# Performance work log

Measured on AMD Instinct MI355X. Metric: run time of the kernel, lower is better.

The kernel has to match this reference:

```python
import jax, jax.numpy as jnp
import numpy as np

H, D, K, FF = 4, 256, 1024, 1024  # n_head, d_model, key_feature_dim, dim_feedforward
L, B = 2048, 4                    # pixels, batch


def setup_inputs() -> dict:
    key = jax.random.key(0)
    ks = jax.random.split(key, 12)
    def g(k, shape, s=0.02):
        return jax.random.normal(k, shape, jnp.float32) * s
    return dict(
        src=jax.random.normal(ks[0], (L, B, D), jnp.float32),
        WK=g(ks[1], (H, K, D), (2.0 / K) ** 0.5),
        WQ=g(ks[2], (H, K, D), (2.0 / K) ** 0.5),
        WV=g(ks[3], (H, D, D), (2.0 / D) ** 0.5),
        TC=g(ks[4], (H, D, D)),
        ENw1=g(ks[5], (H, FF, D)), ENb1=jnp.zeros((H, FF), jnp.float32),
        ENw2=g(ks[6], (H, D, FF)), ENb2=jnp.zeros((H, D), jnp.float32),
        ENg=jnp.ones((H, D), jnp.float32), ENbeta=jnp.zeros((H, D), jnp.float32),
        Wout=g(ks[7], (D, H * D)),
        L1w=g(ks[8], (FF, D)), L1b=jnp.zeros((FF,), jnp.float32),
        L2w=g(ks[9], (D, FF)), L2b=jnp.zeros((D,), jnp.float32),
        N1g=jnp.ones((D,), jnp.float32), N1b=jnp.zeros((D,), jnp.float32),
        N2g=jnp.ones((D,), jnp.float32), N2b=jnp.zeros((D,), jnp.float32),
    )


def _ln(x, g, b, eps=1e-5):
    m = jnp.mean(x, -1, keepdims=True)
    v = jnp.mean((x - m) ** 2, -1, keepdims=True)
    return (x - m) * jax.lax.rsqrt(v + eps) * g + b


def _l2n(x, eps=1e-12):
    n = jnp.sqrt(jnp.sum(x * x, -1, keepdims=True))
    return x / jnp.maximum(n, eps)


def reference(src, WK, WQ, WV, TC, ENw1, ENb1, ENw2, ENb2, ENg, ENbeta,
              Wout, L1w, L1b, L2w, L2b, N1g, N1b, N2g, N2b):
    # --- RMA: per-head RelationUnit, vectorized over head axis h ---
    wq = _l2n(jnp.einsum('lbd,hkd->hlbk', src, WQ))   # (H,L,B,K), L2-normed
    wk = _l2n(jnp.einsum('lbd,hkd->hlbk', src, WK))
    wv = jnp.einsum('lbd,hed->hlbe', src, WV)         # (H,L,B,D)
    dot = jnp.einsum('hlbk,hmbk->hblm', wq, wk)       # (H,B,Lq,Lk)
    aff = jax.nn.softmax(dot, axis=-1)                 # softmax over keys (temp=1)
    aff = aff / (1e-9 + jnp.sum(aff, axis=2, keepdims=True))  # renorm over QUERY dim (torch dim=1)
    out = jnp.einsum('hblm,hmbe->hlbe', aff, wv)       # (H,L,B,D)
    ru = jax.nn.relu(jnp.einsum('hlbe,hfe->hlbf', src[None] - out, TC))
    # per-head extra TransNonlinear: residual MLP + layernorm
    hid = jax.nn.relu(jnp.einsum('hlbd,hfd->hlbf', ru, ENw1) + ENb1[:, None, None, :])
    s2 = jnp.einsum('hlbf,hdf->hlbd', hid, ENw2) + ENb2[:, None, None, :]
    tn = _ln(ru + s2, ENg[:, None, None, :], ENbeta[:, None, None, :])  # (H,L,B,D)
    concat = jnp.transpose(tn, (1, 2, 0, 3)).reshape(L, B, H * D)
    attn = concat @ Wout.T                              # (L,B,D)
    # --- encoder layer: residual + LN + FFN + LN (dropout = eval identity) ---
    x = _ln(src + attn, N1g, N1b)
    ff = jax.nn.relu(x @ L1w.T + L1b) @ L2w.T + L2b
    return _ln(x + ff, N2g, N2b)
```

## Files before the change

kernel.cpp:

```cpp
#include <hip/hip_runtime.h>
#include <hip/hip_bf16.h>

typedef __hip_bfloat16 bf16;
typedef short s16x8 __attribute__((ext_vector_type(8)));
typedef float f32x4 __attribute__((ext_vector_type(4)));

#ifndef __has_builtin
#define __has_builtin(x) 0
#endif
#if __has_builtin(__builtin_amdgcn_global_load_lds)
#define HAS_GLL 1
#else
#define HAS_GLL 0
#endif

#define HN 4
#define DM 256
#define KF 1024
#define FFD 1024
#define LL 2048
#define BB 4
#define NN (LL * BB)
#define HD (HN * DM)

__device__ __forceinline__ float b2f(unsigned short u) {
    unsigned v = ((unsigned)u) << 16; float f; __builtin_memcpy(&f, &v, 4); return f;
}
__device__ __forceinline__ unsigned short f2b(float f) {
    bf16 b = (bf16)f; unsigned short u; __builtin_memcpy(&u, &b, 2); return u;
}

__device__ __forceinline__ float waveReduceSum(float v) {
    for (int o = 32; o; o >>= 1) v += __shfl_down(v, o, 64);
    return v;
}
__device__ __forceinline__ float waveReduceMax(float v) {
    for (int o = 32; o; o >>= 1) v = fmaxf(v, __shfl_down(v, o, 64));
    return v;
}
__device__ __forceinline__ float blockReduceSum(float v) {
    __shared__ float sh[4];
    v = waveReduceSum(v);
    __syncthreads();
    if ((threadIdx.x & 63) == 0) sh[threadIdx.x >> 6] = v;
    __syncthreads();
    return sh[0] + sh[1] + sh[2] + sh[3];
}
__device__ __forceinline__ float blockReduceMax(float v) {
    __shared__ float sh[4];
    v = waveReduceMax(v);
    __syncthreads();
    if ((threadIdx.x & 63) == 0) sh[threadIdx.x >> 6] = v;
    __syncthreads();
    return fmaxf(fmaxf(sh[0], sh[1]), fmaxf(sh[2], sh[3]));
}

__global__ void sentinel_kernel(float* out, float val) {
    if (threadIdx.x == 0 && blockIdx.x == 0) out[0] = val;
}

#if HAS_GLL
__device__ __forceinline__ void gll16(void* g, void* l) {
    __builtin_amdgcn_global_load_lds(
        (__attribute__((address_space(1))) unsigned int*)g,
        (__attribute__((address_space(3))) unsigned int*)l, 16, 0, 0);
}
#endif

template<int BN>
__global__ __launch_bounds__(256) void gemm_nt(
    const void* __restrict__ A, int aF32, int lda, long sA,
    const void* __restrict__ Bv, int bF32, int ldb, long sB,
    void* __restrict__ C, int cF32, int ldc, long sC,
    int Kc,
    const float* __restrict__ bias, long sBias,
    const void* __restrict__ aux, int auxType, int ldaux, long sAux,
    float accSign, int relu)
{
    constexpr int NI = BN / 32;
    constexpr int WN = BN / 2;
    const int z = blockIdx.z;
    const float* Af = (const float*)A + (long)z * sA;
    const bf16*  Ah = (const bf16*)A + (long)z * sA;
    const float* Bf = (const float*)Bv + (long)z * sB;
    const bf16*  Bh = (const bf16*)Bv + (long)z * sB;
    float* Cf = (float*)C + (long)z * sC;
    bf16*  Ch = (bf16*)C + (long)z * sC;
    const float* biasp = bias ? (bias + (long)z * sBias) : nullptr;
    const float* auxf = (auxType == 1) ? ((const float*)aux + (long)z * sAux) : nullptr;
    const bf16*  auxh = (auxType == 2) ? ((const bf16*)aux + (long)z * sAux) : nullptr;

    __shared__ __align__(16) bf16 As[2][128 * 32];
    __shared__ __align__(16) bf16 Bs[2][BN * 32];

    const int tid = threadIdx.x;
    const int lane = tid & 63;
    const int wv = __builtin_amdgcn_readfirstlane(tid >> 6);
    const int wm = (tid >> 6) & 1;
    const int wn = (tid >> 6) >> 1;
    const int lrow = lane & 15;
    const int quad = lane >> 4;
    const int m0 = blockIdx.x * 128;
    const int n0 = blockIdx.y * BN;
    const int srow = tid >> 1;
    const int scol = (tid & 1) * 16;
    const int drow = wv * 16 + (lane >> 2);
    const int dcol = (lane & 3) * 8;

    f32x4 acc[4][NI] = {};

#if HAS_GLL
    if (!aF32 && !bF32) {
        const int nk = Kc >> 5;
        auto stage = [&](int k0, int buf) {
            const bf16* a0 = Ah + (long)(m0 + drow) * lda + k0 + dcol;
            gll16((void*)a0, (void*)&As[buf][wv * 512]);
            gll16((void*)(a0 + (long)lda * 64), (void*)&As[buf][2048 + wv * 512]);
            const bf16* b0 = Bh + (long)(n0 + drow) * ldb + k0 + dcol;
            gll16((void*)b0, (void*)&Bs[buf][wv * 512]);
            if (BN == 128)
                gll16((void*)(b0 + (long)ldb * 64), (void*)&Bs[buf][2048 + wv * 512]);
        };
        stage(0, 0);
        __syncthreads();
        int cur = 0;
        for (int t = 0; t < nk; ++t) {
            if (t + 1 < nk) stage((t + 1) << 5, cur ^ 1);
            s16x8 af[4], bfg[NI];
#pragma unroll
            for (int mi = 0; mi < 4; mi++)
                af[mi] = *(const s16x8*)&As[cur][(wm * 64 + mi * 16 + lrow) * 32 + quad * 8];
#pragma unroll
            for (int ni = 0; ni < NI; ni++)
                bfg[ni] = *(const s16x8*)&Bs[cur][(wn * WN + ni * 16 + lrow) * 32 + quad * 8];
#pragma unroll
            for (int mi = 0; mi < 4; mi++)
#pragma unroll
                for (int ni = 0; ni < NI; ni++)
                    acc[mi][ni] = __builtin_amdgcn_mfma_f32_16x16x32_bf16(af[mi], bfg[ni], acc[mi][ni], 0, 0, 0);
            __syncthreads();
            cur ^= 1;
        }
    } else
#endif
    {
        for (int k0 = 0; k0 < Kc; k0 += 32) {
            uint4 av0, av1, bv0, bv1;
            if (aF32) {
                const float* ag = Af + (long)(m0 + srow) * lda + k0 + scol;
                ushort t[16];
#pragma unroll
                for (int j = 0; j < 4; j++) {
                    float4 f = *(const float4*)(ag + 4 * j);
                    t[4*j] = f2b(f.x); t[4*j+1] = f2b(f.y); t[4*j+2] = f2b(f.z); t[4*j+3] = f2b(f.w);
                }
                av0 = *(const uint4*)&t[0]; av1 = *(const uint4*)&t[8];
            }
#if !HAS_GLL
            else {
                const bf16* ag = Ah + (long)(m0 + srow) * lda + k0 + scol;
                av0 = *(const uint4*)ag; av1 = *(const uint4*)(ag + 8);
            }
#endif
            if (bF32) {
                if (srow < BN) {
                    const float* bg = Bf + (long)(n0 + srow) * ldb + k0 + scol;
                    ushort t[16];
#pragma unroll
                    for (int j = 0; j < 4; j++) {
                        float4 f = *(const float4*)(bg + 4 * j);
                        t[4*j] = f2b(f.x); t[4*j+1] = f2b(f.y); t[4*j+2] = f2b(f.z); t[4*j+3] = f2b(f.w);
                    }
                    bv0 = *(const uint4*)&t[0]; bv1 = *(const uint4*)&t[8];
                }
            }
#if !HAS_GLL
            else {
                if (srow < BN) {
                    const bf16* bg = Bh + (long)(n0 + srow) * ldb + k0 + scol;
                    bv0 = *(const uint4*)bg; bv1 = *(const uint4*)(bg + 8);
                }
            }
#endif
            __syncthreads();
            if (aF32) {
                *(uint4*)&As[0][srow * 32 + scol] = av0;
                *(uint4*)&As[0][srow * 32 + scol + 8] = av1;
            } else {
#if HAS_GLL
                gll16((void*)(Ah + (long)(m0 + drow) * lda + k0 + dcol), (void*)&As[0][wv * 512]);
                gll16((void*)(Ah + (long)(m0 + 64 + drow) * lda + k0 + dcol), (void*)&As[0][2048 + wv * 512]);
#else
                *(uint4*)&As[0][srow * 32 + scol] = av0;
                *(uint4*)&As[0][srow * 32 + scol + 8] = av1;
#endif
            }
            if (bF32) {
                if (srow < BN) {
                    *(uint4*)&Bs[0][srow * 32 + scol] = bv0;
                    *(uint4*)&Bs[0][srow * 32 + scol + 8] = bv1;
                }
            } else {
#if HAS_GLL
                gll16((void*)(Bh + (long)(n0 + drow) * ldb + k0 + dcol), (void*)&Bs[0][wv * 512]);
                if (BN == 128)
                    gll16((void*)(Bh + (long)(n0 + 64 + drow) * ldb + k0 + dcol), (void*)&Bs[0][2048 + wv * 512]);
#else
                if (srow < BN) {
                    *(uint4*)&Bs[0][srow * 32 + scol] = bv0;
                    *(uint4*)&Bs[0][srow * 32 + scol + 8] = bv1;
                }
#endif
            }
            __syncthreads();

            s16x8 af[4], bfg[NI];
#pragma unroll
            for (int mi = 0; mi < 4; mi++)
                af[mi] = *(const s16x8*)&As[0][(wm * 64 + mi * 16 + lrow) * 32 + quad * 8];
#pragma unroll
            for (int ni = 0; ni < NI; ni++)
                bfg[ni] = *(const s16x8*)&Bs[0][(wn * WN + ni * 16 + lrow) * 32 + quad * 8];
#pragma unroll
            for (int mi = 0; mi < 4; mi++)
#pragma unroll
                for (int ni = 0; ni < NI; ni++)
                    acc[mi][ni] = __builtin_amdgcn_mfma_f32_16x16x32_bf16(af[mi], bfg[ni], acc[mi][ni], 0, 0, 0);
        }
    }

#pragma unroll
    for (int mi = 0; mi < 4; mi++) {
#pragma unroll
        for (int ni = 0; ni < NI; ni++) {
            int col = n0 + wn * WN + ni * 16 + lrow;
            float bvl = biasp ? biasp[col] : 0.0f;
#pragma unroll
            for (int i = 0; i < 4; i++) {
                int row = m0 + wm * 64 + mi * 16 + quad * 4 + i;
                float v = accSign * acc[mi][ni][i] + bvl;
                if (auxType == 1) v += auxf[(long)row * ldaux + col];
                else if (auxType == 2) v += (float)auxh[(long)row * ldaux + col];
                if (relu) v = fmaxf(v, 0.0f);
                if (cF32) Cf[(long)row * ldc + col] = v;
                else Ch[(long)row * ldc + col] = (bf16)v;
            }
        }
    }
}

__global__ __launch_bounds__(256) void cvt4(const float* __restrict__ in, bf16* __restrict__ out, int n4) {
    int i = blockIdx.x * 256 + threadIdx.x;
    if (i < n4) {
        float4 f = ((const float4*)in)[i];
        ushort4 u; u.x = f2b(f.x); u.y = f2b(f.y); u.z = f2b(f.z); u.w = f2b(f.w);
        ((ushort4*)out)[i] = u;
    }
}

struct WCvt {
    const float* in[9];
    bf16* out[9];
    int n4[9];
};
__global__ __launch_bounds__(256) void cvt_weights(WCvt wc) {
    int t = blockIdx.y;
    int n4 = wc.n4[t];
    const float4* in = (const float4*)wc.in[t];
    ushort4* out = (ushort4*)wc.out[t];
    for (int i = blockIdx.x * 256 + threadIdx.x; i < n4; i += gridDim.x * 256) {
        float4 f = in[i];
        ushort4 u; u.x = f2b(f.x); u.y = f2b(f.y); u.z = f2b(f.z); u.w = f2b(f.w);
        out[i] = u;
    }
}

__global__ __launch_bounds__(256) void l2norm_rows(bf16* __restrict__ Q) {
    bf16* q = Q + (long)blockIdx.x * KF;
    ushort4 u = ((ushort4*)q)[threadIdx.x];
    float v0 = b2f(u.x), v1 = b2f(u.y), v2 = b2f(u.z), v3 = b2f(u.w);
    float ss = blockReduceSum(v0 * v0 + v1 * v1 + v2 * v2 + v3 * v3);
    float inv = 1.0f / fmaxf(sqrtf(ss), 1e-12f);
    u.x = f2b(v0 * inv); u.y = f2b(v1 * inv); u.z = f2b(v2 * inv); u.w = f2b(v3 * inv);
    ((ushort4*)q)[threadIdx.x] = u;
}

__global__ __launch_bounds__(256) void softmax_rows(bf16* __restrict__ P) {
    bf16* p = P + (long)blockIdx.x * LL;
    ushort4 a = ((ushort4*)p)[2 * threadIdx.x];
    ushort4 b = ((ushort4*)p)[2 * threadIdx.x + 1];
    float v[8] = {b2f(a.x), b2f(a.y), b2f(a.z), b2f(a.w), b2f(b.x), b2f(b.y), b2f(b.z), b2f(b.w)};
    float mx = -1e30f;
#pragma unroll
    for (int i = 0; i < 8; i++) mx = fmaxf(mx, v[i]);
    mx = blockReduceMax(mx);
    float s = 0.0f;
#pragma unroll
    for (int i = 0; i < 8; i++) { v[i] = __expf(v[i] - mx); s += v[i]; }
    s = blockReduceSum(s);
    float inv = 1.0f / s;
    a.x = f2b(v[0]*inv); a.y = f2b(v[1]*inv); a.z = f2b(v[2]*inv); a.w = f2b(v[3]*inv);
    b.x = f2b(v[4]*inv); b.y = f2b(v[5]*inv); b.z = f2b(v[6]*inv); b.w = f2b(v[7]*inv);
    ((ushort4*)p)[2 * threadIdx.x] = a;
    ((ushort4*)p)[2 * threadIdx.x + 1] = b;
}

__global__ __launch_bounds__(256) void zero_cs(float* __restrict__ cs) {
    cs[blockIdx.x * 256 + threadIdx.x] = 0.0f;
}

__global__ __launch_bounds__(256) void colsum2(const bf16* __restrict__ P, float* __restrict__ cs) {
    int col = blockIdx.x * 256 + threadIdx.x;
    int rc = blockIdx.y;
    int b = blockIdx.z;
    const bf16* p = P + (long)b * LL * LL + (long)rc * 128 * LL + col;
    float s = 0.0f;
#pragma unroll 4
    for (int r = 0; r < 128; r++) s += (float)p[(long)r * LL];
    atomicAdd(&cs[(long)b * LL + col], s);
}

__global__ __launch_bounds__(256) void scale_vt(bf16* __restrict__ vt, const float* __restrict__ cs) {
    int e = blockIdx.x, b = blockIdx.y;
    bf16* row = vt + ((long)b * DM + e) * LL;
    const float* c = cs + (long)b * LL;
#pragma unroll
    for (int i = 0; i < 8; i++) {
        int m = threadIdx.x + i * 256;
        row[m] = (bf16)((float)row[m] / (1e-9f + c[m]));
    }
}

__global__ __launch_bounds__(256) void ln_rows(const bf16* __restrict__ in, void* __restrict__ out,
                                               int outF32,
                                               const float* __restrict__ g, const float* __restrict__ b,
                                               const float* __restrict__ aux) {
    long base = (long)blockIdx.x * 256;
    float v = (float)in[base + threadIdx.x];
    if (aux) v += aux[base + threadIdx.x];
    float mean = blockReduceSum(v) * (1.0f / 256.0f);
    float d = v - mean;
    float var = blockReduceSum(d * d) * (1.0f / 256.0f);
    float o = d * rsqrtf(var + 1e-5f) * g[threadIdx.x] + b[threadIdx.x];
    if (outF32) ((float*)out)[base + threadIdx.x] = o;
    else ((bf16*)out)[base + threadIdx.x] = (bf16)o;
}

__global__ __launch_bounds__(256) void ln_cat(bf16* __restrict__ cat, const float* __restrict__ g,
                                              const float* __restrict__ bb) {
    long n = blockIdx.x;
    int h = blockIdx.y;
    bf16* x = cat + n * HD + (long)h * DM;
    float v = (float)x[threadIdx.x];
    float mean = blockReduceSum(v) * (1.0f / 256.0f);
    float d = v - mean;
    float var = blockReduceSum(d * d) * (1.0f / 256.0f);
    x[threadIdx.x] = (bf16)(d * rsqrtf(var + 1e-5f) * g[h * DM + threadIdx.x] + bb[h * DM + threadIdx.x]);
}

extern "C" void kernel_launch(void* const* d_in, const int* in_sizes, int n_in,
                              void* d_out, int out_size, void* d_ws, size_t ws_size,
                              hipStream_t stream) {
    const float* src  = (const float*)d_in[0];
    const float* WK   = (const float*)d_in[1];
    const float* WQ   = (const float*)d_in[2];
    const float* WV   = (const float*)d_in[3];
    const float* TC   = (const float*)d_in[4];
    const float* ENw1 = (const float*)d_in[5];
    const float* ENb1 = (const float*)d_in[6];
    const float* ENw2 = (const float*)d_in[7];
    const float* ENb2 = (const float*)d_in[8];
    const float* ENg  = (const float*)d_in[9];
    const float* ENbt = (const float*)d_in[10];
    const float* Wout = (const float*)d_in[11];
    const float* L1w  = (const float*)d_in[12];
    const float* L1b  = (const float*)d_in[13];
    const float* L2w  = (const float*)d_in[14];
    const float* L2b  = (const float*)d_in[15];
    const float* N1g  = (const float*)d_in[16];
    const float* N1b  = (const float*)d_in[17];
    const float* N2g  = (const float*)d_in[18];
    const float* N2b  = (const float*)d_in[19];

    const size_t COMPACT_FLOOR = 34700000;
    const size_t FAST_FLOOR  = 92307456;
    const size_t FASTW_FLOOR = 92307456 + 11010048;
    if (ws_size < COMPACT_FLOOR || out_size != NN * DM || n_in != 20) {
        float val;
        if (n_in != 20) val = 32768.0f + (float)n_in;
        else if (out_size != NN * DM) val = 49152.0f;
        else val = 16384.0f + 128.0f * (float)(unsigned)(ws_size >> 20);
        sentinel_kernel<<<1, 64, 0, stream>>>((float*)d_out, val);
        return;
    }

    char* w = (char*)d_ws;
    auto G = [&](const void* A, int aF, int lda, long sA,
                 const void* B, int bF, int ldb, long sB,
                 void* C, int cF, int ldc, long sC,
                 int M, int Nn, int Kc, int nb,
                 const float* bias, long sBias,
                 const void* aux, int auxT, int ldaux, long sAux,
                 float sgn, int relu) {
        gemm_nt<128><<<dim3(M / 128, Nn / 128, nb), dim3(256), 0, stream>>>(
            A, aF, lda, sA, B, bF, ldb, sB, C, cF, ldc, sC, Kc,
            bias, sBias, aux, auxT, ldaux, sAux, sgn, relu);
    };
    auto G64 = [&](const void* A, int aF, int lda, long sA,
                 const void* B, int bF, int ldb, long sB,
                 void* C, int cF, int ldc, long sC,
                 int M, int Nn, int Kc, int nb,
                 const float* bias, long sBias,
                 const void* aux, int auxT, int ldaux, long sAux,
                 float sgn, int relu) {
        gemm_nt<64><<<dim3(M / 128, Nn / 64, nb), dim3(256), 0, stream>>>(
            A, aF, lda, sA, B, bF, ldb, sB, C, cF, ldc, sC, Kc,
            bias, sBias, aux, auxT, ldaux, sAux, sgn, relu);
    };

    if (ws_size >= FAST_FLOOR) {
        bf16*  Sb  = (bf16*)(w + 0);
        bf16*  Q   = (bf16*)(w + 4194304);
        bf16*  K   = (bf16*)(w + 20971520);
        bf16*  Vt  = (bf16*)(w + 37748736);
        bf16*  P   = (bf16*)(w + 41943040);
        bf16*  Su  = (bf16*)(w + 75497472);
        float* Cs  = (float*)(w + 92274688);
        bf16* Ru = Q; bf16* Hid = K; bf16* Cat = P;
        bf16* Attn = Vt; bf16* Xln = Su; bf16* Ffh = Q; bf16* Yp = Vt;

        const int haveWb = (ws_size >= FASTW_FLOOR) ? 1 : 0;
        char* wb = w + 92307456;
        bf16* WKb   = (bf16*)(wb + 0);
        bf16* WQb   = (bf16*)(wb + 2097152);
        bf16* WVb   = (bf16*)(wb + 4194304);
        bf16* TCb   = (bf16*)(wb + 4718592);
        bf16* ENw1b = (bf16*)(wb + 5242880);
        bf16* ENw2b = (bf16*)(wb + 7340032);
        bf16* Woutb = (bf16*)(wb + 9437184);
        bf16* L1wb  = (bf16*)(wb + 9961472);
        bf16* L2wb  = (bf16*)(wb + 10485760);
        if (haveWb) {
            WCvt wc;
            wc.in[0] = WK;   wc.out[0] = WKb;   wc.n4[0] = 262144;
            wc.in[1] = WQ;   wc.out[1] = WQb;   wc.n4[1] = 262144;
            wc.in[2] = WV;   wc.out[2] = WVb;   wc.n4[2] = 65536;
            wc.in[3] = TC;   wc.out[3] = TCb;   wc.n4[3] = 65536;
            wc.in[4] = ENw1; wc.out[4] = ENw1b; wc.n4[4] = 262144;
            wc.in[5] = ENw2; wc.out[5] = ENw2b; wc.n4[5] = 262144;
            wc.in[6] = Wout; wc.out[6] = Woutb; wc.n4[6] = 65536;
            wc.in[7] = L1w;  wc.out[7] = L1wb;  wc.n4[7] = 65536;
            wc.in[8] = L2w;  wc.out[8] = L2wb;  wc.n4[8] = 65536;
            cvt_weights<<<dim3(256, 9), 256, 0, stream>>>(wc);
        }
        const int wF = haveWb ? 0 : 1;
        auto WP = [&](const void* f32p, const void* b16p, long off) {
            return haveWb ? (const void*)((const bf16*)b16p + off)
                          : (const void*)((const float*)f32p + off);
        };

        cvt4<<<2048, 256, 0, stream>>>(src, Sb, NN * DM / 4);

        for (int h = 0; h < HN; h++) {
            G(Sb, 0, DM, 0, WP(WQ, WQb, (long)h * KF * DM), wF, DM, 0, Q, 0, KF, 0,
              NN, KF, DM, 1, nullptr, 0, nullptr, 0, 0, 0, 1.0f, 0);
            G(Sb, 0, DM, 0, WP(WK, WKb, (long)h * KF * DM), wF, DM, 0, K, 0, KF, 0,
              NN, KF, DM, 1, nullptr, 0, nullptr, 0, 0, 0, 1.0f, 0);
            G64(WP(WV, WVb, (long)h * DM * DM), wF, DM, 0, Sb, 0, BB * DM, DM,
              Vt, 0, LL, (long)DM * LL,
              DM, LL, DM, BB, nullptr, 0, nullptr, 0, 0, 0, 1.0f, 0);
            l2norm_rows<<<NN, 256, 0, stream>>>(Q);
            l2norm_rows<<<NN, 256, 0, stream>>>(K);
            G(Q, 0, BB * KF, KF, K, 0, BB * KF, KF, P, 0, LL, (long)LL * LL,
              LL, LL, KF, BB, nullptr, 0, nullptr, 0, 0, 0, 1.0f, 0);
            softmax_rows<<<BB * LL, 256, 0, stream>>>(P);
            zero_cs<<<BB * LL / 256, 256, 0, stream>>>(Cs);
            colsum2<<<dim3(LL / 256, 16, BB), 256, 0, stream>>>(P, Cs);
            scale_vt<<<dim3(DM, BB), 256, 0, stream>>>(Vt, Cs);
            G64(P, 0, LL, (long)LL * LL, Vt, 0, LL, (long)DM * LL,
              Su + (long)h * NN * DM, 0, BB * DM, DM,
              LL, DM, LL, BB, nullptr, 0, Sb, 2, BB * DM, DM, -1.0f, 0);
        }
        G(Su, 0, DM, (long)NN * DM, WP(TC, TCb, 0), wF, DM, (long)DM * DM,
          Ru, 0, DM, (long)NN * DM,
          NN, DM, DM, HN, nullptr, 0, nullptr, 0, 0, 0, 1.0f, 1);
        for (int h = 0; h < HN; h++) {
            G(Ru + (long)h * NN * DM, 0, DM, 0, WP(ENw1, ENw1b, (long)h * FFD * DM), wF, DM, 0,
              Hid, 0, FFD, 0, NN, FFD, DM, 1, ENb1 + (long)h * FFD, 0, nullptr, 0, 0, 0, 1.0f, 1);
            G64(Hid, 0, FFD, 0, WP(ENw2, ENw2b, (long)h * DM * FFD), wF, FFD, 0,
              Cat + (long)h * DM, 0, HD, 0, NN, DM, FFD, 1,
              ENb2 + (long)h * DM, 0, Ru + (long)h * NN * DM, 2, DM, 0, 1.0f, 0);
        }
        ln_cat<<<dim3(NN, HN), 256, 0, stream>>>(Cat, ENg, ENbt);
        G64(Cat, 0, HD, 0, WP(Wout, Woutb, 0), wF, HD, 0, Attn, 0, DM, 0,
          NN, DM, HD, 1, nullptr, 0, nullptr, 0, 0, 0, 1.0f, 0);
        ln_rows<<<NN, 256, 0, stream>>>(Attn, Xln, 0, N1g, N1b, src);
        G(Xln, 0, DM, 0, WP(L1w, L1wb, 0), wF, DM, 0, Ffh, 0, FFD, 0,
          NN, FFD, DM, 1, L1b, 0, nullptr, 0, 0, 0, 1.0f, 1);
        G64(Ffh, 0, FFD, 0, WP(L2w, L2wb, 0), wF, FFD, 0, Yp, 0, DM, 0,
          NN, DM, FFD, 1, L2b, 0, Xln, 2, DM, 0, 1.0f, 0);
        ln_rows<<<NN, 256, 0, stream>>>(Yp, (float*)d_out, 1, N2g, N2b, nullptr);
    } else {
        bf16*  S0 = (bf16*)(w + 0);
        bf16*  S1 = (bf16*)(w + 16777216);
        bf16*  S2 = (bf16*)(w + 20971520);
        bf16*  S3 = (bf16*)(w + 25165824);
        bf16*  S4 = (bf16*)(w + 26214400);
        bf16*  S5 = (bf16*)(w + 30408704);
        float* Cs = (float*)(w + 34603008);

        for (int h = 0; h < HN; h++) {
            for (int b = 0; b < BB; b++) {
                G(src + b * DM, 1, BB * DM, 0, WQ + (long)h * KF * DM, 1, DM, 0,
                  S1, 0, KF, 0, LL, KF, DM, 1, nullptr, 0, nullptr, 0, 0, 0, 1.0f, 0);
                G(src + b * DM, 1, BB * DM, 0, WK + (long)h * KF * DM, 1, DM, 0,
                  S2, 0, KF, 0, LL, KF, DM, 1, nullptr, 0, nullptr, 0, 0, 0, 1.0f, 0);
                G(WV + (long)h * DM * DM, 1, DM, 0, src + b * DM, 1, BB * DM, 0,
                  S3, 0, LL, 0, DM, LL, DM, 1, nullptr, 0, nullptr, 0, 0, 0, 1.0f, 0);
                l2norm_rows<<<LL, 256, 0, stream>>>(S1);
                l2norm_rows<<<LL, 256, 0, stream>>>(S2);
                G(S1, 0, KF, 0, S2, 0, KF, 0, S0, 0, LL, 0,
                  LL, LL, KF, 1, nullptr, 0, nullptr, 0, 0, 0, 1.0f, 0);
                softmax_rows<<<LL, 256, 0, stream>>>(S0);
                zero_cs<<<LL / 256, 256, 0, stream>>>(Cs);
                colsum2<<<dim3(LL / 256, 16, 1), 256, 0, stream>>>(S0, Cs);
                scale_vt<<<dim3(DM, 1), 256, 0, stream>>>(S3, Cs);
                G(S0, 0, LL, 0, S3, 0, LL, 0, S4 + b * DM, 0, BB * DM, 0,
                  LL, DM, LL, 1, nullptr, 0, src + b * DM, 1, BB * DM, 0, -1.0f, 0);
            }
            G(S4, 0, DM, 0, TC + (long)h * DM * DM, 1, DM, 0, S1, 0, DM, 0,
              NN, DM, DM, 1, nullptr, 0, nullptr, 0, 0, 0, 1.0f, 1);
            G(S1, 0, DM, 0, ENw1 + (long)h * FFD * DM, 1, DM, 0, S0, 0, FFD, 0,
              NN, FFD, DM, 1, ENb1 + (long)h * FFD, 0, nullptr, 0, 0, 0, 1.0f, 1);
            G(S0, 0, FFD, 0, ENw2 + (long)h * DM * FFD, 1, FFD, 0, S2, 0, DM, 0,
              NN, DM, FFD, 1, ENb2 + (long)h * DM, 0, S1, 2, DM, 0, 1.0f, 0);
            ln_rows<<<NN, 256, 0, stream>>>(S2, S2, 0, ENg + (long)h * DM, ENbt + (long)h * DM, nullptr);
            G(S2, 0, DM, 0, Wout + (long)h * DM, 1, HD, 0, S5, 0, DM, 0,
              NN, DM, DM, 1, nullptr, 0, (h == 0) ? nullptr : (const void*)S5,
              (h == 0) ? 0 : 2, DM, 0, 1.0f, 0);
        }
        ln_rows<<<NN, 256, 0, stream>>>(S5, S1, 0, N1g, N1b, src);
        G(S1, 0, DM, 0, L1w, 1, DM, 0, S0, 0, FFD, 0,
          NN, FFD, DM, 1, L1b, 0, nullptr, 0, 0, 0, 1.0f, 1);
        G(S0, 0, FFD, 0, L2w, 1, FFD, 0, S2, 0, DM, 0,
          NN, DM, FFD, 1, L2b, 0, S1, 2, DM, 0, 1.0f, 0);
        ln_rows<<<NN, 256, 0, stream>>>(S2, (float*)d_out, 1, N2g, N2b, nullptr);
    }
}
```

Measured before the change: 1.140 ms.

## Add 256x256-tile bf16 MFMA GEMM with direct-to-LDS loads for large GEMMs

Adds a new 512-thread GEMM kernel that computes 256x256 output tiles. It stages A and B straight into swizzled LDS with global_load_lds, double-buffers the K loop and interleaves staging with four MFMA phases under s_setprio. The Q/K projections, the QK^T attention-score GEMM, the TC, ENw1 and L1 GEMMs now use it when bf16 weights are available. The aim is more data reuse per tile and better overlap of loads with compute. In exchange it needs 128 KB of LDS per block, which limits occupancy to one block per CU, and it assumes M and N are multiples of 256 and K is a multiple of 64.

```diff
diff --git a/kernel.cpp b/kernel.cpp
--- a/kernel.cpp
+++ b/kernel.cpp
@@ -64,6 +64,186 @@
     __builtin_amdgcn_global_load_lds(
         (__attribute__((address_space(1))) unsigned int*)g,
         (__attribute__((address_space(3))) unsigned int*)l, 16, 0, 0);
+}
+#endif
+
+#define VMC(n) asm volatile("s_waitcnt vmcnt(" #n ")" ::: "memory")
+#define LGKM0() asm volatile("s_waitcnt lgkmcnt(0)" ::: "memory")
+
+#if HAS_GLL
+__global__ __launch_bounds__(512) void gemm256(
+    const bf16* __restrict__ A, int lda, long sA,
+    const bf16* __restrict__ Bv, int ldb, long sB,
+    void* __restrict__ C, int cF32, int ldc, long sC,
+    int Kc,
+    const float* __restrict__ bias, long sBias,
+    const void* __restrict__ aux, int auxType, int ldaux, long sAux,
+    float accSign, int relu)
+{
+    const int z = blockIdx.z;
+    const bf16* Ah = A + (long)z * sA;
+    const bf16* Bh = Bv + (long)z * sB;
+    float* Cf = (float*)C + (long)z * sC;
+    bf16*  Ch = (bf16*)C + (long)z * sC;
+    const float* biasp = bias ? (bias + (long)z * sBias) : nullptr;
+    const float* auxf = (auxType == 1) ? ((const float*)aux + (long)z * sAux) : nullptr;
+    const bf16*  auxh = (auxType == 2) ? ((const bf16*)aux + (long)z * sAux) : nullptr;
+
+    __shared__ __align__(16) bf16 As[2][256 * 64];
+    __shared__ __align__(16) bf16 Bs[2][256 * 64];
+
+    const int tid  = threadIdx.x;
+    const int lane = tid & 63;
+    const int wid  = __builtin_amdgcn_readfirstlane(tid >> 6);
+    const int wm   = wid >> 2;
+    const int wn   = wid & 3;
+    const int lrow = lane & 15;
+    const int quad = lane >> 4;
+    const int m0 = blockIdx.x * 256;
+    const int n0 = blockIdx.y * 256;
+
+    const int srow8  = wid * 8 + (lane >> 3);
+    const int scolsw = ((lane & 7) * 8) ^ ((srow8 & 12) << 2);
+    const bf16* Aorg = Ah + (long)m0 * lda;
+    const bf16* Borg = Bh + (long)n0 * ldb;
+
+    const int colx = (lane & 12) << 2;
+    const int kc0 = (quad * 8) ^ colx;
+    const int kc1 = (32 + quad * 8) ^ colx;
+
+    f32x4 acc[8][4] = {};
+    s16x8 afr[4][2], bfr[4][2];
+
+    const int nk = Kc >> 6;
+
+    auto stg = [&](const bf16* org, int ld, bf16* lds, int k0, int h) {
+#pragma unroll
+        for (int j = 0; j < 2; j++) {
+            int rl = h * 128 + j * 64 + srow8;
+            gll16((void*)(org + (long)rl * ld + k0 + scolsw),
+                  (void*)(lds + (h * 128 + j * 64 + wid * 8) * 64));
+        }
+    };
+
+    stg(Aorg, lda, As[0], 0, 0); stg(Aorg, lda, As[0], 0, 1);
+    stg(Borg, ldb, Bs[0], 0, 0); stg(Borg, ldb, Bs[0], 0, 1);
+    if (nk > 1) {
+        stg(Aorg, lda, As[1], 64, 0); stg(Aorg, lda, As[1], 64, 1);
+        stg(Borg, ldb, Bs[1], 64, 0); stg(Borg, ldb, Bs[1], 64, 1);
+        VMC(8);
+    } else {
+        VMC(0);
+    }
+    __builtin_amdgcn_s_barrier();
+
+    for (int t = 0; t < nk; ++t) {
+        const int s = t & 1;
+        const bf16* Acur = As[s];
+        const bf16* Bcur = Bs[s];
+        bf16* Anxt = As[s ^ 1];
+        bf16* Bslot = Bs[s];
+        const bool stA = (t >= 1) && (t + 1 < nk);
+        const bool stB = (t + 2 < nk);
+
+#pragma unroll
+        for (int mi = 0; mi < 4; mi++) {
+            int r = (wm * 128 + mi * 16 + lrow) * 64;
+            afr[mi][0] = *(const s16x8*)&Acur[r + kc0];
+            afr[mi][1] = *(const s16x8*)&Acur[r + kc1];
+        }
+#pragma unroll
+        for (int ni = 0; ni < 2; ni++) {
+            int r = (wn * 64 + ni * 16 + lrow) * 64;
+            bfr[ni][0] = *(const s16x8*)&Bcur[r + kc0];
+            bfr[ni][1] = *(const s16x8*)&Bcur[r + kc1];
+        }
+        if (stA) stg(Aorg, lda, Anxt, (t + 1) << 6, 0);
+        __builtin_amdgcn_s_barrier();
+        LGKM0();
+        __builtin_amdgcn_s_setprio(1);
+#pragma unroll
+        for (int mi = 0; mi < 4; mi++)
+#pragma unroll
+            for (int ni = 0; ni < 2; ni++)
+#pragma unroll
+                for (int ks = 0; ks < 2; ks++)
+                    acc[mi][ni] = __builtin_amdgcn_mfma_f32_16x16x32_bf16(afr[mi][ks], bfr[ni][ks], acc[mi][ni], 0, 0, 0);
+        __builtin_amdgcn_s_setprio(0);
+        __builtin_amdgcn_s_barrier();
+
+#pragma unroll
+        for (int ni = 0; ni < 2; ni++) {
+            int r = (wn * 64 + (2 + ni) * 16 + lrow) * 64;
+            bfr[2 + ni][0] = *(const s16x8*)&Bcur[r + kc0];
+            bfr[2 + ni][1] = *(const s16x8*)&Bcur[r + kc1];
+        }
+        if (stA) stg(Aorg, lda, Anxt, (t + 1) << 6, 1);
+        __builtin_amdgcn_s_barrier();
+        LGKM0();
+        __builtin_amdgcn_s_setprio(1);
+#pragma unroll
+        for (int mi = 0; mi < 4; mi++)
+#pragma unroll
+            for (int ni = 0; ni < 2; ni++)
+#pragma unroll
+                for (int ks = 0; ks < 2; ks++)
+                    acc[mi][2 + ni] = __builtin_amdgcn_mfma_f32_16x16x32_bf16(afr[mi][ks], bfr[2 + ni][ks], acc[mi][2 + ni], 0, 0, 0);
+        __builtin_amdgcn_s_setprio(0);
+        __builtin_amdgcn_s_barrier();
+
+#pragma unroll
+        for (int mi = 0; mi < 4; mi++) {
+            int r = (wm * 128 + 64 + mi * 16 + lrow) * 64;
+            afr[mi][0] = *(const s16x8*)&Acur[r + kc0];
+            afr[mi][1] = *(const s16x8*)&Acur[r + kc1];
+        }
+        if (stB) stg(Borg, ldb, Bslot, (t + 2) << 6, 0);
+        __builtin_amdgcn_s_barrier();
+        LGKM0();
+        __builtin_amdgcn_s_setprio(1);
+#pragma unroll
+        for (int mi = 0; mi < 4; mi++)
+#pragma unroll
+            for (int ni = 0; ni < 2; ni++)
+#pragma unroll
+                for (int ks = 0; ks < 2; ks++)
+                    acc[4 + mi][ni] = __builtin_amdgcn_mfma_f32_16x16x32_bf16(afr[mi][ks], bfr[ni][ks], acc[4 + mi][ni], 0, 0, 0);
+        __builtin_amdgcn_s_setprio(0);
+        __builtin_amdgcn_s_barrier();
+
+        if (stB) stg(Borg, ldb, Bslot, (t + 2) << 6, 1);
+        __builtin_amdgcn_s_barrier();
+        __builtin_amdgcn_s_setprio(1);
+#pragma unroll
+        for (int mi = 0; mi < 4; mi++)
+#pragma unroll
+            for (int ni = 0; ni < 2; ni++)
+#pragma unroll
+                for (int ks = 0; ks < 2; ks++)
+                    acc[4 + mi][2 + ni] = __builtin_amdgcn_mfma_f32_16x16x32_bf16(afr[mi][ks], bfr[2 + ni][ks], acc[4 + mi][2 + ni], 0, 0, 0);
+        __builtin_amdgcn_s_setprio(0);
+        if (stB) { VMC(4); } else { VMC(0); }
+        __builtin_amdgcn_s_barrier();
+    }
+
+#pragma unroll
+    for (int mi = 0; mi < 8; mi++) {
+#pragma unroll
+        for (int ni = 0; ni < 4; ni++) {
+            int col = n0 + wn * 64 + ni * 16 + lrow;
+            float bvl = biasp ? biasp[col] : 0.0f;
+#pragma unroll
+            for (int i = 0; i < 4; i++) {
+                int row = m0 + wm * 128 + mi * 16 + quad * 4 + i;
+                float v = accSign * acc[mi][ni][i] + bvl;
+                if (auxType == 1) v += auxf[(long)row * ldaux + col];
+                else if (auxType == 2) v += (float)auxh[(long)row * ldaux + col];
+                if (relu) v = fmaxf(v, 0.0f);
+                if (cF32) Cf[(long)row * ldc + col] = v;
+                else Ch[(long)row * ldc + col] = (bf16)v;
+            }
+        }
+    }
 }
 #endif
 
@@ -417,6 +597,19 @@
             A, aF, lda, sA, B, bF, ldb, sB, C, cF, ldc, sC, Kc,
             bias, sBias, aux, auxT, ldaux, sAux, sgn, relu);
     };
+#if HAS_GLL
+    auto G2 = [&](const void* A, int lda, long sA,
+                  const void* B, int ldb, long sB,
+                  void* C, int cF, int ldc, long sC,
+                  int M, int Nn, int Kc, int nb,
+                  const float* bias, long sBias,
+                  const void* aux, int auxT, int ldaux, long sAux,
+                  float sgn, int relu) {
+        gemm256<<<dim3(M / 256, Nn / 256, nb), dim3(512), 0, stream>>>(
+            (const bf16*)A, lda, sA, (const bf16*)B, ldb, sB, C, cF, ldc, sC, Kc,
+            bias, sBias, aux, auxT, ldaux, sAux, sgn, relu);
+    };
+#endif
 
     if (ws_size >= FAST_FLOOR) {
         bf16*  Sb  = (bf16*)(w + 0);
@@ -462,17 +655,32 @@
         cvt4<<<2048, 256, 0, stream>>>(src, Sb, NN * DM / 4);
 
         for (int h = 0; h < HN; h++) {
-            G(Sb, 0, DM, 0, WP(WQ, WQb, (long)h * KF * DM), wF, DM, 0, Q, 0, KF, 0,
-              NN, KF, DM, 1, nullptr, 0, nullptr, 0, 0, 0, 1.0f, 0);
-            G(Sb, 0, DM, 0, WP(WK, WKb, (long)h * KF * DM), wF, DM, 0, K, 0, KF, 0,
-              NN, KF, DM, 1, nullptr, 0, nullptr, 0, 0, 0, 1.0f, 0);
+#if HAS_GLL
+            if (haveWb) {
+                G2(Sb, DM, 0, WQb + (long)h * KF * DM, DM, 0, Q, 0, KF, 0,
+                   NN, KF, DM, 1, nullptr, 0, nullptr, 0, 0, 0, 1.0f, 0);
+                G2(Sb, DM, 0, WKb + (long)h * KF * DM, DM, 0, K, 0, KF, 0,
+                   NN, KF, DM, 1, nullptr, 0, nullptr, 0, 0, 0, 1.0f, 0);
+            } else
+#endif
+            {
+                G(Sb, 0, DM, 0, WP(WQ, WQb, (long)h * KF * DM), wF, DM, 0, Q, 0, KF, 0,
+                  NN, KF, DM, 1, nullptr, 0, nullptr, 0, 0, 0, 1.0f, 0);
+                G(Sb, 0, DM, 0, WP(WK, WKb, (long)h * KF * DM), wF, DM, 0, K, 0, KF, 0,
+                  NN, KF, DM, 1, nullptr, 0, nullptr, 0, 0, 0, 1.0f, 0);
+            }
             G64(WP(WV, WVb, (long)h * DM * DM), wF, DM, 0, Sb, 0, BB * DM, DM,
               Vt, 0, LL, (long)DM * LL,
               DM, LL, DM, BB, nullptr, 0, nullptr, 0, 0, 0, 1.0f, 0);
             l2norm_rows<<<NN, 256, 0, stream>>>(Q);
             l2norm_rows<<<NN, 256, 0, stream>>>(K);
+#if HAS_GLL
+            G2(Q, BB * KF, KF, K, BB * KF, KF, P, 0, LL, (long)LL * LL,
+               LL, LL, KF, BB, nullptr, 0, nullptr, 0, 0, 0, 1.0f, 0);
+#else
             G(Q, 0, BB * KF, KF, K, 0, BB * KF, KF, P, 0, LL, (long)LL * LL,
               LL, LL, KF, BB, nullptr, 0, nullptr, 0, 0, 0, 1.0f, 0);
+#endif
             softmax_rows<<<BB * LL, 256, 0, stream>>>(P);
             zero_cs<<<BB * LL / 256, 256, 0, stream>>>(Cs);
             colsum2<<<dim3(LL / 256, 16, BB), 256, 0, stream>>>(P, Cs);
@@ -481,12 +689,29 @@
               Su + (long)h * NN * DM, 0, BB * DM, DM,
               LL, DM, LL, BB, nullptr, 0, Sb, 2, BB * DM, DM, -1.0f, 0);
         }
-        G(Su, 0, DM, (long)NN * DM, WP(TC, TCb, 0), wF, DM, (long)DM * DM,
-          Ru, 0, DM, (long)NN * DM,
-          NN, DM, DM, HN, nullptr, 0, nullptr, 0, 0, 0, 1.0f, 1);
+#if HAS_GLL
+        if (haveWb) {
+            G2(Su, DM, (long)NN * DM, TCb, DM, (long)DM * DM,
+               Ru, 0, DM, (long)NN * DM,
+               NN, DM, DM, HN, nullptr, 0, nullptr, 0, 0, 0, 1.0f, 1);
+        } else
+#endif
+        {
+            G(Su, 0, DM, (long)NN * DM, WP(TC, TCb, 0), wF, DM, (long)DM * DM,
+              Ru, 0, DM, (long)NN * DM,
+              NN, DM, DM, HN, nullptr, 0, nullptr, 0, 0, 0, 1.0f, 1);
+        }
         for (int h = 0; h < HN; h++) {
-            G(Ru + (long)h * NN * DM, 0, DM, 0, WP(ENw1, ENw1b, (long)h * FFD * DM), wF, DM, 0,
-              Hid, 0, FFD, 0, NN, FFD, DM, 1, ENb1 + (long)h * FFD, 0, nullptr, 0, 0, 0, 1.0f, 1);
+#if HAS_GLL
+            if (haveWb) {
+                G2(Ru + (long)h * NN * DM, DM, 0, ENw1b + (long)h * FFD * DM, DM, 0,
+                   Hid, 0, FFD, 0, NN, FFD, DM, 1, ENb1 + (long)h * FFD, 0, nullptr, 0, 0, 0, 1.0f, 1);
+            } else
+#endif
+            {
+                G(Ru + (long)h * NN * DM, 0, DM, 0, WP(ENw1, ENw1b, (long)h * FFD * DM), wF, DM, 0,
+                  Hid, 0, FFD, 0, NN, FFD, DM, 1, ENb1 + (long)h * FFD, 0, nullptr, 0, 0, 0, 1.0f, 1);
+            }
             G64(Hid, 0, FFD, 0, WP(ENw2, ENw2b, (long)h * DM * FFD), wF, FFD, 0,
               Cat + (long)h * DM, 0, HD, 0, NN, DM, FFD, 1,
               ENb2 + (long)h * DM, 0, Ru + (long)h * NN * DM, 2, DM, 0, 1.0f, 0);
@@ -495,8 +720,16 @@
         G64(Cat, 0, HD, 0, WP(Wout, Woutb, 0), wF, HD, 0, Attn, 0, DM, 0,
           NN, DM, HD, 1, nullptr, 0, nullptr, 0, 0, 0, 1.0f, 0);
         ln_rows<<<NN, 256, 0, stream>>>(Attn, Xln, 0, N1g, N1b, src);
-        G(Xln, 0, DM, 0, WP(L1w, L1wb, 0), wF, DM, 0, Ffh, 0, FFD, 0,
-          NN, FFD, DM, 1, L1b, 0, nullptr, 0, 0, 0, 1.0f, 1);
+#if HAS_GLL
+        if (haveWb) {
+            G2(Xln, DM, 0, L1wb, DM, 0, Ffh, 0, FFD, 0,
+               NN, FFD, DM, 1, L1b, 0, nullptr, 0, 0, 0, 1.0f, 1);
+        } else
+#endif
+        {
+            G(Xln, 0, DM, 0, WP(L1w, L1wb, 0), wF, DM, 0, Ffh, 0, FFD, 0,
+              NN, FFD, DM, 1, L1b, 0, nullptr, 0, 0, 0, 1.0f, 1);
+        }
         G64(Ffh, 0, FFD, 0, WP(L2w, L2wb, 0), wF, FFD, 0, Yp, 0, DM, 0,
           NN, DM, FFD, 1, L2b, 0, Xln, 2, DM, 0, 1.0f, 0);
         ln_rows<<<NN, 256, 0, stream>>>(Yp, (float*)d_out, 1, N2g, N2b, nullptr);
```

Measured after the change: 1.146 ms. No clear change (+0.6%).
